# Optimization experiments

Hardware: AMD Instinct MI355X
Metric: run time of the kernel (lower is better)

Reference implementation:

```python
import jax, jax.numpy as jnp
import numpy as np

DIM = 2048
NUM_HEADS = 16
HEAD_DIM = DIM // NUM_HEADS  # 128
SEQ_LEN = 2048
ROPE_THETA = 10000.0


def _rope_tables(T, head_dim, dtype=jnp.float32):
    inv_freq = 1.0 / (ROPE_THETA ** (jnp.arange(0, head_dim, 2, dtype=jnp.float32) / head_dim))
    t = jnp.arange(T, dtype=jnp.float32)
    freqs = jnp.outer(t, inv_freq)  # [T, head_dim//2]
    return jnp.cos(freqs).astype(dtype), jnp.sin(freqs).astype(dtype)


def setup_inputs() -> dict:
    key = jax.random.key(0)
    ks = jax.random.split(key, 9)
    s = 1.0 / jnp.sqrt(DIM)
    x = jax.random.normal(ks[0], (SEQ_LEN, DIM), dtype=jnp.float32)
    wq = jax.random.uniform(ks[1], (DIM, DIM), minval=-s, maxval=s, dtype=jnp.float32)
    wk = jax.random.uniform(ks[2], (DIM, DIM), minval=-s, maxval=s, dtype=jnp.float32)
    wv = jax.random.uniform(ks[3], (DIM, DIM), minval=-s, maxval=s, dtype=jnp.float32)
    wp = jax.random.uniform(ks[4], (DIM, DIM), minval=-s, maxval=s, dtype=jnp.float32)
    bq = jax.random.uniform(ks[5], (DIM,), minval=-s, maxval=s, dtype=jnp.float32)
    bk = jax.random.uniform(ks[6], (DIM,), minval=-s, maxval=s, dtype=jnp.float32)
    bv = jax.random.uniform(ks[7], (DIM,), minval=-s, maxval=s, dtype=jnp.float32)
    bp = jax.random.uniform(ks[8], (DIM,), minval=-s, maxval=s, dtype=jnp.float32)
    cos, sin = _rope_tables(SEQ_LEN, HEAD_DIM)
    return {"x": x, "wq": wq, "bq": bq, "wk": wk, "bk": bk, "wv": wv, "bv": bv,
            "wp": wp, "bp": bp, "cos": cos, "sin": sin}


def _apply_rope(t, cos, sin):
    # t: [T, H, D]; cos/sin: [T, D//2]
    T, H, D = t.shape
    tr = t.reshape(T, H, D // 2, 2)
    r, i = tr[..., 0], tr[..., 1]
    c = cos[:, None, :]
    s = sin[:, None, :]
    out = jnp.stack([r * c - i * s, r * s + i * c], axis=-1)
    return out.reshape(T, H, D)


def reference(x, wq, bq, wk, bk, wv, bv, wp, bp, cos, sin):
    T, C = x.shape
    H, D = NUM_HEADS, C // NUM_HEADS
    q = (x @ wq.T + bq).reshape(T, H, D)
    k = (x @ wk.T + bk).reshape(T, H, D)
    v = (x @ wv.T + bv).reshape(T, H, D)
    q = _apply_rope(q, cos, sin)
    k = _apply_rope(k, cos, sin)
    # scores: [H, T, T]; NOTE: source scales by full dim C, not head_dim
    attn = jnp.einsum('thd,shd->hts', q, k) * (C ** -0.5)
    mask = jnp.tril(jnp.ones((T, T), dtype=bool))
    attn = jnp.where(mask[None], attn, -jnp.inf)
    attn = jax.nn.softmax(attn, axis=-1)
    out = jnp.einsum('hts,shd->thd', attn, v).reshape(T, C)
    return out @ wp.T + bp
```

## Files before the change

### kernel.cpp

```cpp
#include <hip/hip_runtime.h>
#include <math.h>

typedef __attribute__((ext_vector_type(8))) short  bf16x8;
typedef __attribute__((ext_vector_type(4))) float  f32x4;
typedef __attribute__((ext_vector_type(8))) ushort u16x8;
typedef __attribute__((ext_vector_type(4))) ushort u16x4;

#define SEQ   2048
#define CDIM  2048
#define NHEAD 16
#define DHEAD 128
#define SCALE 0.02209708691207961f
#define LOG2E 1.4426950408889634f

__device__ __forceinline__ ushort f2bf(float f) {
    uint u = __float_as_uint(f);
    u += 0x7FFFu + ((u >> 16) & 1u);
    return (ushort)(u >> 16);
}
__device__ __forceinline__ float bf2f(ushort h) {
    return __uint_as_float(((uint)h) << 16);
}

#define GLOAD16(gsrc, ldst)                                                  \
    __builtin_amdgcn_global_load_lds(                                        \
        (const __attribute__((address_space(1))) void*)(gsrc),               \
        (__attribute__((address_space(3))) void*)(ldst), 16, 0, 0)

__global__ __launch_bounds__(256) void f2bf_kernel(const float* __restrict__ src,
                                                   ushort* __restrict__ dst, int n8)
{
    const int i = blockIdx.x * 256 + threadIdx.x;
    if (i >= n8) return;
    const float4 a = ((const float4*)src)[i * 2];
    const float4 b = ((const float4*)src)[i * 2 + 1];
    u16x8 o;
    o[0] = f2bf(a.x); o[1] = f2bf(a.y); o[2] = f2bf(a.z); o[3] = f2bf(a.w);
    o[4] = f2bf(b.x); o[5] = f2bf(b.y); o[6] = f2bf(b.z); o[7] = f2bf(b.w);
    *(u16x8*)&dst[(size_t)i * 8] = o;
}

__global__ __launch_bounds__(256) void f2bf3_kernel(const float* __restrict__ s0,
                                                    const float* __restrict__ s1,
                                                    const float* __restrict__ s2,
                                                    ushort* __restrict__ d0,
                                                    ushort* __restrict__ d1,
                                                    ushort* __restrict__ d2)
{
    const int z = blockIdx.y;
    const float* src = z == 0 ? s0 : z == 1 ? s1 : s2;
    ushort*      dst = z == 0 ? d0 : z == 1 ? d1 : d2;
    const int i = blockIdx.x * 256 + threadIdx.x;
    const float4 a = ((const float4*)src)[i * 2];
    const float4 b = ((const float4*)src)[i * 2 + 1];
    u16x8 o;
    o[0] = f2bf(a.x); o[1] = f2bf(a.y); o[2] = f2bf(a.z); o[3] = f2bf(a.w);
    o[4] = f2bf(b.x); o[5] = f2bf(b.y); o[6] = f2bf(b.z); o[7] = f2bf(b.w);
    *(u16x8*)&dst[(size_t)i * 8] = o;
}

__global__ __launch_bounds__(256) void gemm_nt_mfma_f32(const ushort* __restrict__ A,
                                                        const ushort* __restrict__ B,
                                                        const float* __restrict__ bias,
                                                        float* __restrict__ outp)
{
    __shared__ ushort As[128 * 32];
    __shared__ ushort Bs[128 * 32];
    const int tid  = threadIdx.x;
    const int lane = tid & 63, wid = tid >> 6;
    const int wr = wid >> 1, wc = wid & 1;
    const int l4 = lane >> 4, l15 = lane & 15;
    const int m0 = blockIdx.y * 128, n0 = blockIdx.x * 128;

    f32x4 acc[4][4];
    #pragma unroll
    for (int i = 0; i < 4; ++i)
        #pragma unroll
        for (int j = 0; j < 4; ++j) acc[i][j] = 0.f;

    const int srow = wid * 32 + (lane >> 2);
    const int scol = (lane & 3) * 8;

    for (int k0 = 0; k0 < CDIM; k0 += 32) {
        __syncthreads();
        GLOAD16(&A[(size_t)(m0 + srow)      * CDIM + k0 + scol], (char*)As + wid * 2048);
        GLOAD16(&A[(size_t)(m0 + srow + 16) * CDIM + k0 + scol], (char*)As + wid * 2048 + 1024);
        GLOAD16(&B[(size_t)(n0 + srow)      * CDIM + k0 + scol], (char*)Bs + wid * 2048);
        GLOAD16(&B[(size_t)(n0 + srow + 16) * CDIM + k0 + scol], (char*)Bs + wid * 2048 + 1024);
        __syncthreads();

        bf16x8 af[4], bfr[4];
        #pragma unroll
        for (int f = 0; f < 4; ++f) {
            af[f]  = *(const bf16x8*)&As[(wr * 64 + f * 16 + l15) * 32 + l4 * 8];
            bfr[f] = *(const bf16x8*)&Bs[(wc * 64 + f * 16 + l15) * 32 + l4 * 8];
        }
        #pragma unroll
        for (int i = 0; i < 4; ++i)
            #pragma unroll
            for (int j = 0; j < 4; ++j)
                acc[i][j] = __builtin_amdgcn_mfma_f32_16x16x32_bf16(af[i], bfr[j], acc[i][j], 0, 0, 0);
    }

    float bn[4];
    #pragma unroll
    for (int j = 0; j < 4; ++j) bn[j] = bias[n0 + wc * 64 + j * 16 + l15];

    #pragma unroll
    for (int i = 0; i < 4; ++i)
        #pragma unroll
        for (int j = 0; j < 4; ++j) {
            const int n = n0 + wc * 64 + j * 16 + l15;
            #pragma unroll
            for (int r = 0; r < 4; ++r) {
                const int m = m0 + wr * 64 + i * 16 + l4 * 4 + r;
                outp[(size_t)m * CDIM + n] = acc[i][j][r] + bn[j];
            }
        }
}

__global__ __launch_bounds__(256) void gemm_qkv(const ushort* __restrict__ A,
                                                const ushort* __restrict__ W0,
                                                const ushort* __restrict__ W1,
                                                const ushort* __restrict__ W2,
                                                const float* __restrict__ b0,
                                                const float* __restrict__ b1,
                                                const float* __restrict__ b2,
                                                ushort* __restrict__ o0,
                                                ushort* __restrict__ o1,
                                                ushort* __restrict__ o2)
{
    __shared__ ushort As[128 * 32];
    __shared__ ushort Bs[128 * 32];
    const int z = blockIdx.z;
    const ushort* B    = z == 0 ? W0 : z == 1 ? W1 : W2;
    const float*  bias = z == 0 ? b0 : z == 1 ? b1 : b2;

    const int tid  = threadIdx.x;
    const int lane = tid & 63, wid = tid >> 6;
    const int wr = wid >> 1, wc = wid & 1;
    const int l4 = lane >> 4, l15 = lane & 15;
    const int m0 = blockIdx.y * 128, n0 = blockIdx.x * 128;

    f32x4 acc[4][4];
    #pragma unroll
    for (int i = 0; i < 4; ++i)
        #pragma unroll
        for (int j = 0; j < 4; ++j) acc[i][j] = 0.f;

    const int srow = wid * 32 + (lane >> 2);
    const int scol = (lane & 3) * 8;

    for (int k0 = 0; k0 < CDIM; k0 += 32) {
        __syncthreads();
        GLOAD16(&A[(size_t)(m0 + srow)      * CDIM + k0 + scol], (char*)As + wid * 2048);
        GLOAD16(&A[(size_t)(m0 + srow + 16) * CDIM + k0 + scol], (char*)As + wid * 2048 + 1024);
        GLOAD16(&B[(size_t)(n0 + srow)      * CDIM + k0 + scol], (char*)Bs + wid * 2048);
        GLOAD16(&B[(size_t)(n0 + srow + 16) * CDIM + k0 + scol], (char*)Bs + wid * 2048 + 1024);
        __syncthreads();

        bf16x8 af[4], bfr[4];
        #pragma unroll
        for (int f = 0; f < 4; ++f) {
            af[f]  = *(const bf16x8*)&As[(wr * 64 + f * 16 + l15) * 32 + l4 * 8];
            bfr[f] = *(const bf16x8*)&Bs[(wc * 64 + f * 16 + l15) * 32 + l4 * 8];
        }
        #pragma unroll
        for (int i = 0; i < 4; ++i)
            #pragma unroll
            for (int j = 0; j < 4; ++j)
                acc[i][j] = __builtin_amdgcn_mfma_f32_16x16x32_bf16(af[i], bfr[j], acc[i][j], 0, 0, 0);
    }

    float bn[4];
    #pragma unroll
    for (int j = 0; j < 4; ++j) bn[j] = bias[n0 + wc * 64 + j * 16 + l15];

    if (z == 2) {
        #pragma unroll
        for (int i = 0; i < 4; ++i)
            #pragma unroll
            for (int j = 0; j < 4; ++j) {
                const int n = n0 + wc * 64 + j * 16 + l15;
                const int mb = m0 + wr * 64 + i * 16 + l4 * 4;
                u16x4 pk;
                #pragma unroll
                for (int r = 0; r < 4; ++r) pk[r] = f2bf(acc[i][j][r] + bn[j]);
                *(u16x4*)&o2[(size_t)n * SEQ + mb] = pk;
            }
    } else {
        ushort* outp = z == 0 ? o0 : o1;
        #pragma unroll
        for (int i = 0; i < 4; ++i)
            #pragma unroll
            for (int j = 0; j < 4; ++j) {
                const int n = n0 + wc * 64 + j * 16 + l15;
                #pragma unroll
                for (int r = 0; r < 4; ++r) {
                    const int m = m0 + wr * 64 + i * 16 + l4 * 4 + r;
                    outp[(size_t)m * CDIM + n] = f2bf(acc[i][j][r] + bn[j]);
                }
            }
    }
}

__global__ __launch_bounds__(256) void rope_bf16(ushort* __restrict__ q, ushort* __restrict__ k,
                                                 const float* __restrict__ cosT,
                                                 const float* __restrict__ sinT)
{
    const int idx = blockIdx.x * 256 + threadIdx.x;
    ushort* buf = blockIdx.y ? k : q;
    const int base = idx * 8;
    const int t   = base >> 11;
    const int fi0 = (base & 127) >> 1;
    const float4 c4 = *(const float4*)&cosT[t * 64 + fi0];
    const float4 s4 = *(const float4*)&sinT[t * 64 + fi0];
    const float c[4] = {c4.x, c4.y, c4.z, c4.w};
    const float s[4] = {s4.x, s4.y, s4.z, s4.w};
    u16x8 v = *(const u16x8*)&buf[base];
    u16x8 o;
    #pragma unroll
    for (int p = 0; p < 4; ++p) {
        const float r  = bf2f(v[2 * p]);
        const float im = bf2f(v[2 * p + 1]);
        o[2 * p]     = f2bf(r * c[p] - im * s[p]);
        o[2 * p + 1] = f2bf(r * s[p] + im * c[p]);
    }
    *(u16x8*)&buf[base] = o;
}

__global__ __launch_bounds__(256) void flash_attn_mfma(const ushort* __restrict__ qb,
                                                       const ushort* __restrict__ kb,
                                                       const ushort* __restrict__ vT,
                                                       ushort* __restrict__ ao)
{
    __shared__ ushort Ks[64 * 136];
    __shared__ ushort VTs[128 * 72];
    __shared__ float  S_lds[64 * 68];
    __shared__ ushort Ps[64 * 72];
    __shared__ float  rowM[64], rowL[64], rowF[64];

    const int tid  = threadIdx.x;
    const int lane = tid & 63, wid = tid >> 6;
    const int wr = wid >> 1, wc = wid & 1;
    const int l4 = lane >> 4, l15 = lane & 15;
    const int h = blockIdx.y;
    const int qt = gridDim.x - 1 - blockIdx.x;
    const int q0 = qt * 64;

    if (tid < 64) { rowM[tid] = -INFINITY; rowL[tid] = 0.f; }

    bf16x8 qf[2][4];
    #pragma unroll
    for (int fm = 0; fm < 2; ++fm)
        #pragma unroll
        for (int ks = 0; ks < 4; ++ks) {
            const int row = q0 + wr * 32 + fm * 16 + l15;
            const int col = h * DHEAD + ks * 32 + l4 * 8;
            qf[fm][ks] = *(const bf16x8*)&qb[(size_t)row * CDIM + col];
        }

    f32x4 acc_o[2][4];
    #pragma unroll
    for (int fm = 0; fm < 2; ++fm)
        #pragma unroll
        for (int fn = 0; fn < 4; ++fn) acc_o[fm][fn] = 0.f;

    for (int kt = 0; kt <= qt; ++kt) {
        __syncthreads();

        #pragma unroll
        for (int i2 = 0; i2 < 4; ++i2) {
            const int r  = (tid >> 4) + i2 * 16;
            const int c8 = (tid & 15) * 8;
            *(u16x8*)&Ks[r * 136 + c8] =
                *(const u16x8*)&kb[(size_t)(kt * 64 + r) * CDIM + h * DHEAD + c8];
        }
        #pragma unroll
        for (int i2 = 0; i2 < 4; ++i2) {
            const int r  = (tid >> 3) + i2 * 32;
            const int c8 = (tid & 7) * 8;
            *(u16x8*)&VTs[r * 72 + c8] =
                *(const u16x8*)&vT[(size_t)(h * DHEAD + r) * SEQ + kt * 64 + c8];
        }
        __syncthreads();

        f32x4 sacc[2][2];
        #pragma unroll
        for (int fm = 0; fm < 2; ++fm)
            #pragma unroll
            for (int fn = 0; fn < 2; ++fn) sacc[fm][fn] = 0.f;
        #pragma unroll
        for (int ks = 0; ks < 4; ++ks) {
            bf16x8 kf[2];
            #pragma unroll
            for (int fn = 0; fn < 2; ++fn)
                kf[fn] = *(const bf16x8*)&Ks[(wc * 32 + fn * 16 + l15) * 136 + ks * 32 + l4 * 8];
            #pragma unroll
            for (int fm = 0; fm < 2; ++fm)
                #pragma unroll
                for (int fn = 0; fn < 2; ++fn)
                    sacc[fm][fn] = __builtin_amdgcn_mfma_f32_16x16x32_bf16(qf[fm][ks], kf[fn], sacc[fm][fn], 0, 0, 0);
        }
        #pragma unroll
        for (int fm = 0; fm < 2; ++fm)
            #pragma unroll
            for (int fn = 0; fn < 2; ++fn)
                #pragma unroll
                for (int r = 0; r < 4; ++r) {
                    const int srow = wr * 32 + fm * 16 + l4 * 4 + r;
                    const int scol = wc * 32 + fn * 16 + l15;
                    float sv = sacc[fm][fn][r] * SCALE;
                    if (kt == qt && scol > srow) sv = -INFINITY;
                    S_lds[srow * 68 + scol] = sv;
                }
        __syncthreads();

        {
            const int srow = tid >> 2;
            const int c0   = (tid & 3) * 16;
            float vals[16];
            #pragma unroll
            for (int c = 0; c < 16; ++c) vals[c] = S_lds[srow * 68 + c0 + c];
            float mt = vals[0];
            #pragma unroll
            for (int c = 1; c < 16; ++c) mt = fmaxf(mt, vals[c]);
            mt = fmaxf(mt, __shfl_xor(mt, 1));
            mt = fmaxf(mt, __shfl_xor(mt, 2));
            const float mold = rowM[srow];
            const float mnew = fmaxf(mold, mt);
            float sum = 0.f;
            ushort pb[16];
            #pragma unroll
            for (int c = 0; c < 16; ++c) {
                const float p = exp2f((vals[c] - mnew) * LOG2E);
                sum += p;
                pb[c] = f2bf(p);
            }
            sum += __shfl_xor(sum, 1);
            sum += __shfl_xor(sum, 2);
            u16x8 w0, w1;
            #pragma unroll
            for (int c = 0; c < 8; ++c) { w0[c] = pb[c]; w1[c] = pb[c + 8]; }
            *(u16x8*)&Ps[srow * 72 + c0]     = w0;
            *(u16x8*)&Ps[srow * 72 + c0 + 8] = w1;
            if ((tid & 3) == 0) {
                const float fac = exp2f((mold - mnew) * LOG2E);
                rowF[srow] = fac;
                rowL[srow] = rowL[srow] * fac + sum;
                rowM[srow] = mnew;
            }
        }
        __syncthreads();

        float frv[2][4];
        #pragma unroll
        for (int fm = 0; fm < 2; ++fm)
            #pragma unroll
            for (int r = 0; r < 4; ++r)
                frv[fm][r] = rowF[wr * 32 + fm * 16 + l4 * 4 + r];
        #pragma unroll
        for (int fm = 0; fm < 2; ++fm)
            #pragma unroll
            for (int fn = 0; fn < 4; ++fn)
                #pragma unroll
                for (int r = 0; r < 4; ++r) acc_o[fm][fn][r] *= frv[fm][r];

        #pragma unroll
        for (int ks = 0; ks < 2; ++ks) {
            bf16x8 pa[2];
            #pragma unroll
            for (int fm = 0; fm < 2; ++fm)
                pa[fm] = *(const bf16x8*)&Ps[(wr * 32 + fm * 16 + l15) * 72 + ks * 32 + l4 * 8];
            #pragma unroll
            for (int fn = 0; fn < 4; ++fn) {
                bf16x8 vf = *(const bf16x8*)&VTs[(wc * 64 + fn * 16 + l15) * 72 + ks * 32 + l4 * 8];
                #pragma unroll
                for (int fm = 0; fm < 2; ++fm)
                    acc_o[fm][fn] = __builtin_amdgcn_mfma_f32_16x16x32_bf16(pa[fm], vf, acc_o[fm][fn], 0, 0, 0);
            }
        }
    }

    #pragma unroll
    for (int fm = 0; fm < 2; ++fm)
        #pragma unroll
        for (int r = 0; r < 4; ++r) {
            const int lrow = wr * 32 + fm * 16 + l4 * 4 + r;
            const float invl = 1.f / rowL[lrow];
            #pragma unroll
            for (int fn = 0; fn < 4; ++fn) {
                const int gcol = h * DHEAD + wc * 64 + fn * 16 + l15;
                ao[(size_t)(q0 + lrow) * CDIM + gcol] = f2bf(acc_o[fm][fn][r] * invl);
            }
        }
}

extern "C" void kernel_launch(void* const* d_in, const int* in_sizes, int n_in,
                              void* d_out, int out_size, void* d_ws, size_t ws_size,
                              hipStream_t stream) {
    const float* x    = (const float*)d_in[0];
    const float* wq   = (const float*)d_in[1];
    const float* bq   = (const float*)d_in[2];
    const float* wk   = (const float*)d_in[3];
    const float* bk   = (const float*)d_in[4];
    const float* wv   = (const float*)d_in[5];
    const float* bv   = (const float*)d_in[6];
    const float* wp   = (const float*)d_in[7];
    const float* bp   = (const float*)d_in[8];
    const float* cosT = (const float*)d_in[9];
    const float* sinT = (const float*)d_in[10];

    const size_t mat = (size_t)SEQ * CDIM;
    ushort* xb  = (ushort*)d_ws;
    ushort* w0  = xb  + mat;
    ushort* w1  = w0  + mat;
    ushort* w2  = w1  + mat;
    ushort* qbb = w2  + mat;
    ushort* kbb = qbb + mat;
    ushort* vTb = kbb + mat;
    ushort* aob = w0;

    const int n8 = (int)(mat / 8);
    const dim3 cgrid(n8 / 256);

    f2bf_kernel<<<cgrid, 256, 0, stream>>>(x, xb, n8);
    f2bf3_kernel<<<dim3(n8 / 256, 3), 256, 0, stream>>>(wq, wk, wv, w0, w1, w2);

    gemm_qkv<<<dim3(16, 16, 3), 256, 0, stream>>>(xb, w0, w1, w2, bq, bk, bv,
                                                  qbb, kbb, vTb);

    rope_bf16<<<dim3(SEQ * CDIM / 8 / 256, 2), 256, 0, stream>>>(qbb, kbb, cosT, sinT);

    flash_attn_mfma<<<dim3(SEQ / 64, NHEAD), 256, 0, stream>>>(qbb, kbb, vTb, aob);

    f2bf_kernel<<<cgrid, 256, 0, stream>>>(wp, w1, n8);
    gemm_nt_mfma_f32<<<dim3(16, 16), 256, 0, stream>>>(aob, w1, bp, (float*)d_out);

    (void)in_sizes; (void)n_in; (void)out_size; (void)ws_size;
}
```

Measured before the change: 351.5 us.

## Fuse RoPE into QKV GEMM epilogue, merge casts, prefetch K/V in flash attention

Applies RoPE inside the QKV GEMM epilogue, using a lane shuffle to fetch the paired element, which removes the separate rope kernel and its extra read/write pass over Q and K. All five fp32-to-bf16 conversions are merged into one launch. Flash attention now register-prefetches the next K/V tile while the current tile's scores are computed. The trade-offs are extra cos/sin loads in the epilogue, more register pressure in attention, and one more bf16 weight buffer in workspace.

```diff
diff --git a/kernel.cpp b/kernel.cpp
--- a/kernel.cpp
+++ b/kernel.cpp
@@ -27,29 +27,17 @@
         (const __attribute__((address_space(1))) void*)(gsrc),               \
         (__attribute__((address_space(3))) void*)(ldst), 16, 0, 0)
 
-__global__ __launch_bounds__(256) void f2bf_kernel(const float* __restrict__ src,
-                                                   ushort* __restrict__ dst, int n8)
-{
-    const int i = blockIdx.x * 256 + threadIdx.x;
-    if (i >= n8) return;
-    const float4 a = ((const float4*)src)[i * 2];
-    const float4 b = ((const float4*)src)[i * 2 + 1];
-    u16x8 o;
-    o[0] = f2bf(a.x); o[1] = f2bf(a.y); o[2] = f2bf(a.z); o[3] = f2bf(a.w);
-    o[4] = f2bf(b.x); o[5] = f2bf(b.y); o[6] = f2bf(b.z); o[7] = f2bf(b.w);
-    *(u16x8*)&dst[(size_t)i * 8] = o;
-}
-
-__global__ __launch_bounds__(256) void f2bf3_kernel(const float* __restrict__ s0,
-                                                    const float* __restrict__ s1,
-                                                    const float* __restrict__ s2,
-                                                    ushort* __restrict__ d0,
-                                                    ushort* __restrict__ d1,
-                                                    ushort* __restrict__ d2)
+__global__ __launch_bounds__(256) void f2bf5_kernel(
+    const float* __restrict__ s0, const float* __restrict__ s1,
+    const float* __restrict__ s2, const float* __restrict__ s3,
+    const float* __restrict__ s4,
+    ushort* __restrict__ d0, ushort* __restrict__ d1,
+    ushort* __restrict__ d2, ushort* __restrict__ d3,
+    ushort* __restrict__ d4)
 {
     const int z = blockIdx.y;
-    const float* src = z == 0 ? s0 : z == 1 ? s1 : s2;
-    ushort*      dst = z == 0 ? d0 : z == 1 ? d1 : d2;
+    const float* src = z == 0 ? s0 : z == 1 ? s1 : z == 2 ? s2 : z == 3 ? s3 : s4;
+    ushort*      dst = z == 0 ? d0 : z == 1 ? d1 : z == 2 ? d2 : z == 3 ? d3 : d4;
     const int i = blockIdx.x * 256 + threadIdx.x;
     const float4 a = ((const float4*)src)[i * 2];
     const float4 b = ((const float4*)src)[i * 2 + 1];
@@ -126,6 +114,8 @@
                                                 const float* __restrict__ b0,
                                                 const float* __restrict__ b1,
                                                 const float* __restrict__ b2,
+                                                const float* __restrict__ cosT,
+                                                const float* __restrict__ sinT,
                                                 ushort* __restrict__ o0,
                                                 ushort* __restrict__ o1,
                                                 ushort* __restrict__ o2)
@@ -194,39 +184,22 @@
         for (int i = 0; i < 4; ++i)
             #pragma unroll
             for (int j = 0; j < 4; ++j) {
-                const int n = n0 + wc * 64 + j * 16 + l15;
+                const int n  = n0 + wc * 64 + j * 16 + l15;
+                const int fi = (n & 127) >> 1;
+                const bool odd = (n & 1) != 0;
                 #pragma unroll
                 for (int r = 0; r < 4; ++r) {
                     const int m = m0 + wr * 64 + i * 16 + l4 * 4 + r;
-                    outp[(size_t)m * CDIM + n] = f2bf(acc[i][j][r] + bn[j]);
+                    const float val     = acc[i][j][r] + bn[j];
+                    const float partner = __shfl_xor(val, 1);
+                    const float c = cosT[m * 64 + fi];
+                    const float s = sinT[m * 64 + fi];
+                    const float res = odd ? (partner * s + val * c)
+                                          : (val * c - partner * s);
+                    outp[(size_t)m * CDIM + n] = f2bf(res);
                 }
             }
     }
-}
-
-__global__ __launch_bounds__(256) void rope_bf16(ushort* __restrict__ q, ushort* __restrict__ k,
-                                                 const float* __restrict__ cosT,
-                                                 const float* __restrict__ sinT)
-{
-    const int idx = blockIdx.x * 256 + threadIdx.x;
-    ushort* buf = blockIdx.y ? k : q;
-    const int base = idx * 8;
-    const int t   = base >> 11;
-    const int fi0 = (base & 127) >> 1;
-    const float4 c4 = *(const float4*)&cosT[t * 64 + fi0];
-    const float4 s4 = *(const float4*)&sinT[t * 64 + fi0];
-    const float c[4] = {c4.x, c4.y, c4.z, c4.w};
-    const float s[4] = {s4.x, s4.y, s4.z, s4.w};
-    u16x8 v = *(const u16x8*)&buf[base];
-    u16x8 o;
-    #pragma unroll
-    for (int p = 0; p < 4; ++p) {
-        const float r  = bf2f(v[2 * p]);
-        const float im = bf2f(v[2 * p + 1]);
-        o[2 * p]     = f2bf(r * c[p] - im * s[p]);
-        o[2 * p + 1] = f2bf(r * s[p] + im * c[p]);
-    }
-    *(u16x8*)&buf[base] = o;
 }
 
 __global__ __launch_bounds__(256) void flash_attn_mfma(const ushort* __restrict__ qb,
@@ -266,23 +239,26 @@
         #pragma unroll
         for (int fn = 0; fn < 4; ++fn) acc_o[fm][fn] = 0.f;
 
+    const int rK = tid >> 4,  cK = (tid & 15) * 8;
+    const int rV = tid >> 3,  cV = (tid & 7) * 8;
+    u16x8 kreg[4], vreg[4];
+
+    #pragma unroll
+    for (int i2 = 0; i2 < 4; ++i2)
+        kreg[i2] = *(const u16x8*)&kb[(size_t)(rK + i2 * 16) * CDIM + h * DHEAD + cK];
+    #pragma unroll
+    for (int i2 = 0; i2 < 4; ++i2)
+        vreg[i2] = *(const u16x8*)&vT[(size_t)(h * DHEAD + rV + i2 * 32) * SEQ + cV];
+
     for (int kt = 0; kt <= qt; ++kt) {
         __syncthreads();
 
         #pragma unroll
-        for (int i2 = 0; i2 < 4; ++i2) {
-            const int r  = (tid >> 4) + i2 * 16;
-            const int c8 = (tid & 15) * 8;
-            *(u16x8*)&Ks[r * 136 + c8] =
-                *(const u16x8*)&kb[(size_t)(kt * 64 + r) * CDIM + h * DHEAD + c8];
-        }
-        #pragma unroll
-        for (int i2 = 0; i2 < 4; ++i2) {
-            const int r  = (tid >> 3) + i2 * 32;
-            const int c8 = (tid & 7) * 8;
-            *(u16x8*)&VTs[r * 72 + c8] =
-                *(const u16x8*)&vT[(size_t)(h * DHEAD + r) * SEQ + kt * 64 + c8];
-        }
+        for (int i2 = 0; i2 < 4; ++i2)
+            *(u16x8*)&Ks[(rK + i2 * 16) * 136 + cK] = kreg[i2];
+        #pragma unroll
+        for (int i2 = 0; i2 < 4; ++i2)
+            *(u16x8*)&VTs[(rV + i2 * 32) * 72 + cV] = vreg[i2];
         __syncthreads();
 
         f32x4 sacc[2][2];
@@ -302,6 +278,16 @@
                 for (int fn = 0; fn < 2; ++fn)
                     sacc[fm][fn] = __builtin_amdgcn_mfma_f32_16x16x32_bf16(qf[fm][ks], kf[fn], sacc[fm][fn], 0, 0, 0);
         }
+
+        if (kt < qt) {
+            #pragma unroll
+            for (int i2 = 0; i2 < 4; ++i2)
+                kreg[i2] = *(const u16x8*)&kb[(size_t)((kt + 1) * 64 + rK + i2 * 16) * CDIM + h * DHEAD + cK];
+            #pragma unroll
+            for (int i2 = 0; i2 < 4; ++i2)
+                vreg[i2] = *(const u16x8*)&vT[(size_t)(h * DHEAD + rV + i2 * 32) * SEQ + (kt + 1) * 64 + cV];
+        }
+
         #pragma unroll
         for (int fm = 0; fm < 2; ++fm)
             #pragma unroll
@@ -416,26 +402,23 @@
     ushort* w0  = xb  + mat;
     ushort* w1  = w0  + mat;
     ushort* w2  = w1  + mat;
-    ushort* qbb = w2  + mat;
+    ushort* w3  = w2  + mat;
+    ushort* qbb = w3  + mat;
     ushort* kbb = qbb + mat;
     ushort* vTb = kbb + mat;
-    ushort* aob = w0;
+    ushort* aob = xb;
 
     const int n8 = (int)(mat / 8);
-    const dim3 cgrid(n8 / 256);
-
-    f2bf_kernel<<<cgrid, 256, 0, stream>>>(x, xb, n8);
-    f2bf3_kernel<<<dim3(n8 / 256, 3), 256, 0, stream>>>(wq, wk, wv, w0, w1, w2);
+
+    f2bf5_kernel<<<dim3(n8 / 256, 5), 256, 0, stream>>>(x, wq, wk, wv, wp,
+                                                        xb, w0, w1, w2, w3);
 
     gemm_qkv<<<dim3(16, 16, 3), 256, 0, stream>>>(xb, w0, w1, w2, bq, bk, bv,
-                                                  qbb, kbb, vTb);
-
-    rope_bf16<<<dim3(SEQ * CDIM / 8 / 256, 2), 256, 0, stream>>>(qbb, kbb, cosT, sinT);
+                                                  cosT, sinT, qbb, kbb, vTb);
 
     flash_attn_mfma<<<dim3(SEQ / 64, NHEAD), 256, 0, stream>>>(qbb, kbb, vTb, aob);
 
-    f2bf_kernel<<<cgrid, 256, 0, stream>>>(wp, w1, n8);
-    gemm_nt_mfma_f32<<<dim3(16, 16), 256, 0, stream>>>(aob, w1, bp, (float*)d_out);
+    gemm_nt_mfma_f32<<<dim3(16, 16), 256, 0, stream>>>(aob, w3, bp, (float*)d_out);
 
     (void)in_sizes; (void)n_in; (void)out_size; (void)ws_size;
 }
```

New measurement: 344.2 us. -2.1%, faster.
